# Optimization experiments

Measured on AMD Instinct MI355X. Metric: run time of the kernel, lower is better.

Reference implementation:

```python
import jax, jax.numpy as jnp
import numpy as np

NEG = -1e9


def setup_inputs() -> dict:
    key = jax.random.key(0)
    k1, k2, k3, k4 = jax.random.split(key, 4)
    R, N, D = 64, 200000, 256
    hs = jax.random.normal(k1, (R, D), dtype=jnp.float32)
    es = jax.random.normal(k2, (N, D), dtype=jnp.float32)
    W = jax.random.normal(k3, (D, D), dtype=jnp.float32) / np.sqrt(D)
    mask = jax.random.randint(k4, (R, N), 0, 2) > 0
    return {"hs": hs, "es": es, "W": W, "mask": mask, "n_output": 50}


def reference(hs, es, W, mask, n_output):
    # MatchingLayer: bilinear match scores[r, n] = hs_r^T W es_n  -> [R, N]
    original_scores = (hs @ W) @ es.T
    mu = original_scores.mean()
    std = original_scores.std(ddof=1)  # torch .std() is unbiased
    scores = (original_scores - mu) / std
    # logits used for expansion scores (differentiable)
    logits = jax.nn.log_softmax(scores, axis=-1) + jax.nn.log_softmax(scores, axis=0)
    # detached probabilities for selection
    d = jax.lax.stop_gradient(scores)
    row_probs = jnp.maximum(jax.nn.softmax(jnp.where(mask, d, NEG), axis=-1), 1e-6)
    col_probs = jnp.maximum(jax.nn.softmax(jnp.where(mask, d, NEG), axis=0), 1e-6)
    # deterministic (eval) path: assign each candidate to its argmax category
    index = jnp.argmax(col_probs, axis=0)  # [N]
    R = scores.shape[0]
    valid = mask & (index[None, :] == jnp.arange(R)[:, None])  # [R, N]
    sel = jnp.where(valid, row_probs, -jnp.inf)
    top_vals, top_idx = jax.lax.top_k(sel, n_output)  # [R, n_output]
    ok = jnp.isfinite(top_vals)  # rows with fewer candidates than n_output -> padded
    expansions = jnp.where(ok, top_idx, -1)  # [R, n_output], -1 = pad
    # expansion_scores[i] = logits[:, expansion_i].T -> [n_output, R]
    exp_scores = jnp.transpose(logits[:, top_idx], (1, 2, 0))  # [R, n_output, R]
    exp_scores = exp_scores * ok[:, :, None].astype(exp_scores.dtype)
    return expansions, exp_scores
```

## Files before the change

### kernel.cpp

```cpp
#include <hip/hip_runtime.h>
#include <math.h>

#define RR 64
#define DD 256
#define CAP 6144


__device__ __forceinline__ void get_mu_istd(const double* sums, int N, float& fmu, float& istd) {
  double M = (double)RR * (double)N;
  double mu = sums[0] / M;
  double var = (sums[1] - sums[0] * sums[0] / M) / (M - 1.0);
  fmu = (float)mu;
  istd = (float)(1.0 / sqrt(var));
}

__device__ __forceinline__ void cp16(const void* g, void* l) {
  __builtin_amdgcn_global_load_lds((const __attribute__((address_space(1))) void*)g,
                                   (__attribute__((address_space(3))) void*)l, 16, 0, 0);
}


__global__ __launch_bounds__(256) void k_mask(const void* __restrict__ maskp,
                                              unsigned long long* __restrict__ mbits,
                                              int N) {
  __shared__ int f;
  __shared__ unsigned short pb[4][256];
  int tid = threadIdx.x;
  if (tid == 0) f = 0;
  __syncthreads();
  {
    const unsigned* mw = (const unsigned*)maskp;
    int mode = 0;
    for (int i = tid; i < 4096; i += 256) {
      unsigned v = mw[i];
      if (v == 0x3f800000u) mode = 2;
      else if (v > 1u && mode != 2) mode = 1;
    }
    if (mode) atomicMax(&f, mode);
  }
  __syncthreads();
  const int mode = f;

  const int lane = tid & 63, ty = tid >> 6;
  const int R0 = ty * 16;
  const int n0 = blockIdx.x * 256;
  const int n4 = n0 + lane * 4;
  unsigned g0 = 0, g1 = 0, g2 = 0, g3 = 0;
  const bool vec_ok = (n4 + 3) < N;

  if (mode == 1) {
    const unsigned char* m = (const unsigned char*)maskp;
    if (vec_ok) {
#pragma unroll
      for (int i = 0; i < 16; ++i) {
        uchar4 v = *(const uchar4*)(m + (size_t)(R0 + i) * N + n4);
        g0 |= (unsigned)(v.x != 0) << i;
        g1 |= (unsigned)(v.y != 0) << i;
        g2 |= (unsigned)(v.z != 0) << i;
        g3 |= (unsigned)(v.w != 0) << i;
      }
    } else {
      unsigned* gp[4] = {&g0, &g1, &g2, &g3};
      for (int c = 0; c < 4; ++c)
        if (n4 + c < N)
          for (int i = 0; i < 16; ++i)
            *gp[c] |= (unsigned)(m[(size_t)(R0 + i) * N + n4 + c] != 0) << i;
    }
  } else if (mode == 2) {
    const float* m = (const float*)maskp;
    if (vec_ok) {
#pragma unroll
      for (int i = 0; i < 16; ++i) {
        float4 v = *(const float4*)(m + (size_t)(R0 + i) * N + n4);
        g0 |= (unsigned)(v.x != 0.f) << i;
        g1 |= (unsigned)(v.y != 0.f) << i;
        g2 |= (unsigned)(v.z != 0.f) << i;
        g3 |= (unsigned)(v.w != 0.f) << i;
      }
    } else {
      unsigned* gp[4] = {&g0, &g1, &g2, &g3};
      for (int c = 0; c < 4; ++c)
        if (n4 + c < N)
          for (int i = 0; i < 16; ++i)
            *gp[c] |= (unsigned)(m[(size_t)(R0 + i) * N + n4 + c] != 0.f) << i;
    }
  } else {
    const int* m = (const int*)maskp;
    if (vec_ok) {
#pragma unroll
      for (int i = 0; i < 16; ++i) {
        int4 v = *(const int4*)(m + (size_t)(R0 + i) * N + n4);
        g0 |= (unsigned)(v.x != 0) << i;
        g1 |= (unsigned)(v.y != 0) << i;
        g2 |= (unsigned)(v.z != 0) << i;
        g3 |= (unsigned)(v.w != 0) << i;
      }
    } else {
      unsigned* gp[4] = {&g0, &g1, &g2, &g3};
      for (int c = 0; c < 4; ++c)
        if (n4 + c < N)
          for (int i = 0; i < 16; ++i)
            *gp[c] |= (unsigned)(m[(size_t)(R0 + i) * N + n4 + c] != 0) << i;
    }
  }
  pb[ty][lane * 4 + 0] = (unsigned short)g0;
  pb[ty][lane * 4 + 1] = (unsigned short)g1;
  pb[ty][lane * 4 + 2] = (unsigned short)g2;
  pb[ty][lane * 4 + 3] = (unsigned short)g3;
  __syncthreads();
  const int n = n0 + tid;
  if (n < N) {
    mbits[n] = (unsigned long long)pb[0][tid] |
               ((unsigned long long)pb[1][tid] << 16) |
               ((unsigned long long)pb[2][tid] << 32) |
               ((unsigned long long)pb[3][tid] << 48);
  }
}


__global__ __launch_bounds__(256) void k_hsw(const float* __restrict__ hs,
                                             const float* __restrict__ W,
                                             float* __restrict__ hsW) {
  int i = blockIdx.x;
  int j = threadIdx.x;
  float acc = 0.f;
  for (int k = 0; k < DD; ++k) acc = fmaf(hs[i * DD + k], W[k * DD + j], acc);
  hsW[i * DD + j] = acc;
}


__global__ __launch_bounds__(256) void k_scores(const float* __restrict__ es,
                                                const float* __restrict__ hsW,
                                                const unsigned long long* __restrict__ mbits,
                                                float* __restrict__ scores,
                                                float* __restrict__ colmax,
                                                int* __restrict__ colargmax,
                                                float* __restrict__ qpart,
                                                double* __restrict__ spart,
                                                int N) {
  __shared__ float lds[20480];
  const int tid = threadIdx.x;
  const int lane = tid & 63;
  const int ty = __builtin_amdgcn_readfirstlane(tid >> 6);
  const int n0 = blockIdx.x * 256;
  const int R0 = ty * 16;
  const int nb = n0 + lane;

  const int srow = ty * 8 + (lane >> 3);
  const int sg4 = (((lane & 7) ^ ((lane >> 3) & 7)) << 2);
  const int wrow = ty * 16 + (lane >> 2);
  const int wg4 = (lane & 3) << 2;

  float4 acc[16];
#pragma unroll
  for (int i = 0; i < 16; ++i) acc[i] = make_float4(0.f, 0.f, 0.f, 0.f);

  auto stage = [&](float* ebase, float* wbase, int kc) {
#pragma unroll
    for (int p = 0; p < 8; ++p) {
      const int col = p * 32 + srow;
      const int rr = min(n0 + col, N - 1);
      cp16(es + (size_t)rr * DD + kc + sg4, ebase + p * 1024 + ty * 256);
    }
    cp16(hsW + (size_t)wrow * DD + kc + wg4, wbase + ty * 256);
    cp16(hsW + (size_t)wrow * DD + kc + 16 + wg4, wbase + 1024 + ty * 256);
  };

  stage(lds, lds + 16384, 0);
  asm volatile("s_waitcnt vmcnt(0)" ::: "memory");
  __syncthreads();

  const int swz = (lane & 7);

  for (int kc = 0; kc < DD; kc += 32) {
    const int cur = (kc >> 5) & 1;
    float* ebC = lds + (cur ? 8192 : 0);
    float* wbC = lds + 16384 + (cur ? 2048 : 0);
    if (kc + 32 < DD) {
      float* ebN = lds + (cur ? 0 : 8192);
      float* wbN = lds + 16384 + (cur ? 0 : 2048);
      stage(ebN, wbN, kc + 32);
    }
#pragma unroll
    for (int k = 0; k < 32; k += 4) {
      const int eswz = (((k >> 2) ^ swz) << 2);
      const float4 e0 = *(const float4*)(ebC + (lane       ) * 32 + eswz);
      const float4 e1 = *(const float4*)(ebC + (lane +  64 ) * 32 + eswz);
      const float4 e2 = *(const float4*)(ebC + (lane + 128 ) * 32 + eswz);
      const float4 e3 = *(const float4*)(ebC + (lane + 192 ) * 32 + eswz);
      const float* wk = wbC + ((k >> 4) * 1024) + (k & 15);
#pragma unroll
      for (int i = 0; i < 16; ++i) {
        const float4 w = *(const float4*)(wk + (R0 + i) * 16);
        acc[i].x = fmaf(w.x, e0.x, fmaf(w.y, e0.y, fmaf(w.z, e0.z, fmaf(w.w, e0.w, acc[i].x))));
        acc[i].y = fmaf(w.x, e1.x, fmaf(w.y, e1.y, fmaf(w.z, e1.z, fmaf(w.w, e1.w, acc[i].y))));
        acc[i].z = fmaf(w.x, e2.x, fmaf(w.y, e2.y, fmaf(w.z, e2.z, fmaf(w.w, e2.w, acc[i].z))));
        acc[i].w = fmaf(w.x, e3.x, fmaf(w.y, e3.y, fmaf(w.z, e3.z, fmaf(w.w, e3.w, acc[i].w))));
      }
    }
    asm volatile("s_waitcnt vmcnt(0)" ::: "memory");
    __syncthreads();
  }

  bool val[4];
#pragma unroll
  for (int c = 0; c < 4; ++c) val[c] = (nb + 64 * c) < N;

#pragma unroll
  for (int i = 0; i < 16; ++i) {
    float* dst = scores + (size_t)(R0 + i) * N + nb;
    float v[4] = {acc[i].x, acc[i].y, acc[i].z, acc[i].w};
#pragma unroll
    for (int c = 0; c < 4; ++c)
      if (val[c]) dst[64 * c] = v[c];
  }

  unsigned long long mb[4];
#pragma unroll
  for (int c = 0; c < 4; ++c) mb[c] = val[c] ? mbits[nb + 64 * c] : 0ull;

  float ps1[4], ps2[4], pcm[4], pbv[4];
  int pbr[4];
#pragma unroll
  for (int c = 0; c < 4; ++c) { ps1[c] = 0.f; ps2[c] = 0.f; pcm[c] = -INFINITY; pbv[c] = -INFINITY; pbr[c] = -1; }

#pragma unroll
  for (int i = 0; i < 16; ++i) {
    const int rrow = R0 + i;
    float v[4] = {acc[i].x, acc[i].y, acc[i].z, acc[i].w};
    float q = -INFINITY, qm = -INFINITY;
#pragma unroll
    for (int c = 0; c < 4; ++c) {
      ps1[c] += v[c];
      ps2[c] = fmaf(v[c], v[c], ps2[c]);
      pcm[c] = fmaxf(pcm[c], v[c]);
      bool bit = (mb[c] >> rrow) & 1ull;
      if (bit && (v[c] > pbv[c])) { pbv[c] = v[c]; pbr[c] = rrow; }
      float qv = val[c] ? v[c] : -INFINITY;
      q = fmaxf(q, qv);
      if (bit) qm = fmaxf(qm, qv);
    }
#pragma unroll
    for (int o = 32; o > 0; o >>= 1) {
      q = fmaxf(q, __shfl_down(q, o));
      qm = fmaxf(qm, __shfl_down(qm, o));
    }
    if (lane == 0) {
      qpart[(size_t)blockIdx.x * 128 + rrow] = q;
      qpart[(size_t)blockIdx.x * 128 + 64 + rrow] = qm;
    }
  }

  __syncthreads();
  float* Ls1 = lds;
  float* Ls2 = lds + 1024;
  float* Lcm = lds + 2048;
  float* Lbv = lds + 3072;
  int* Lbr = (int*)(lds + 4096);
  double* red = (double*)(lds + 5120);
#pragma unroll
  for (int c = 0; c < 4; ++c) {
    int col = lane + 64 * c;
    Ls1[ty * 256 + col] = ps1[c];
    Ls2[ty * 256 + col] = ps2[c];
    Lcm[ty * 256 + col] = pcm[c];
    Lbv[ty * 256 + col] = pbv[c];
    Lbr[ty * 256 + col] = pbr[c];
  }
  __syncthreads();

  const int n = n0 + tid;
  float s1 = 0.f, s2 = 0.f;
  if (n < N) {
    s1 = Ls1[tid] + Ls1[256 + tid] + Ls1[512 + tid] + Ls1[768 + tid];
    s2 = Ls2[tid] + Ls2[256 + tid] + Ls2[512 + tid] + Ls2[768 + tid];
    float cm = fmaxf(fmaxf(Lcm[tid], Lcm[256 + tid]), fmaxf(Lcm[512 + tid], Lcm[768 + tid]));
    colmax[n] = cm;
    float bv = -INFINITY;
    int br = -1;
#pragma unroll
    for (int w2 = 0; w2 < 4; ++w2) {
      float b = Lbv[w2 * 256 + tid];
      if (b > bv) { bv = b; br = Lbr[w2 * 256 + tid]; }
    }
    colargmax[n] = br;
  }

  double d1 = (double)s1, d2 = (double)s2;
#pragma unroll
  for (int o = 32; o > 0; o >>= 1) {
    d1 += __shfl_down(d1, o);
    d2 += __shfl_down(d2, o);
  }
  if ((tid & 63) == 0) { red[ty * 2] = d1; red[ty * 2 + 1] = d2; }
  __syncthreads();
  if (tid == 0) {
    spart[(size_t)blockIdx.x * 2] = red[0] + red[2] + red[4] + red[6];
    spart[(size_t)blockIdx.x * 2 + 1] = red[1] + red[3] + red[5] + red[7];
  }
}


__global__ __launch_bounds__(256) void k_redfuse(const float* __restrict__ qpart,
                                                 const double* __restrict__ spart,
                                                 float* __restrict__ rowmaxf,
                                                 double* __restrict__ sums,
                                                 int* __restrict__ cnt,
                                                 int NBlk) {
  const int tid = threadIdx.x, lane = tid & 63, ty = tid >> 6;
  if (blockIdx.x < 128) {
    const int slot = blockIdx.x;
    __shared__ float w[4];
    float m = -INFINITY;
    for (int i = tid; i < NBlk; i += 256) m = fmaxf(m, qpart[(size_t)i * 128 + slot]);
#pragma unroll
    for (int o = 32; o > 0; o >>= 1) m = fmaxf(m, __shfl_down(m, o));
    if (lane == 0) w[ty] = m;
    __syncthreads();
    if (tid == 0) rowmaxf[slot] = fmaxf(fmaxf(w[0], w[1]), fmaxf(w[2], w[3]));
  } else {
    __shared__ double r[8];
    double s0 = 0.0, s1 = 0.0;
    for (int i = tid; i < NBlk; i += 256) {
      s0 += spart[(size_t)i * 2];
      s1 += spart[(size_t)i * 2 + 1];
    }
#pragma unroll
    for (int o = 32; o > 0; o >>= 1) {
      s0 += __shfl_down(s0, o);
      s1 += __shfl_down(s1, o);
    }
    if (lane == 0) { r[ty * 2] = s0; r[ty * 2 + 1] = s1; }
    if (tid < RR) cnt[tid] = 0;
    __syncthreads();
    if (tid == 0) {
      sums[0] = r[0] + r[2] + r[4] + r[6];
      sums[1] = r[1] + r[3] + r[5] + r[7];
    }
  }
}


__global__ __launch_bounds__(256) void k_colpass(const float* __restrict__ scores,
                                                 const float* __restrict__ colmax,
                                                 const int* __restrict__ colargmax,
                                                 const unsigned long long* __restrict__ mbits,
                                                 const double* __restrict__ sums,
                                                 const float* __restrict__ rowmaxf,
                                                 float* __restrict__ collse,
                                                 float* __restrict__ colpart,
                                                 int* __restrict__ cnt,
                                                 float* __restrict__ candx,
                                                 int* __restrict__ candn,
                                                 int N) {
  __shared__ float rmS[64], suS[64], smS[64];
  __shared__ float rowU[64], rowM[64];
  __shared__ float cpart[4][256];
  __shared__ int lcnt[64], lbase[64];
  const int tid = threadIdx.x, lane = tid & 63, ty = tid >> 6;
  const int R0 = ty * 16;
  float fmu, istd;
  get_mu_istd(sums, N, fmu, istd);
  if (tid < 64) {
    rmS[tid] = rowmaxf[tid];
    lcnt[tid] = 0;
  }
  __syncthreads();
  float gm = rmS[0];
#pragma unroll
  for (int r = 1; r < RR; ++r) gm = fmaxf(gm, rmS[r]);
  if (tid < 64) {
    suS[tid] = expf((gm - rmS[tid]) * istd);
    smS[tid] = expf((gm - rowmaxf[64 + tid]) * istd);
  }

  const int n0 = blockIdx.x * 256;
  const int n4 = n0 + lane * 4;
  bool vc[4];
  unsigned mbr[4];
#pragma unroll
  for (int c = 0; c < 4; ++c) {
    vc[c] = (n4 + c) < N;
    unsigned long long mw = vc[c] ? mbits[n4 + c] : 0ull;
    mbr[c] = (unsigned)((mw >> R0) & 0xffffull);
  }

  float cs0 = 0.f, cs1 = 0.f, cs2 = 0.f, cs3 = 0.f;
#pragma unroll
  for (int i = 0; i < 16; ++i) {
    const int r = R0 + i;
    const float4 x = *(const float4*)(scores + (size_t)r * N + n4);
    float E0 = vc[0] ? expf((x.x - gm) * istd) : 0.f;
    float E1 = vc[1] ? expf((x.y - gm) * istd) : 0.f;
    float E2 = vc[2] ? expf((x.z - gm) * istd) : 0.f;
    float E3 = vc[3] ? expf((x.w - gm) * istd) : 0.f;
    cs0 += E0; cs1 += E1; cs2 += E2; cs3 += E3;
    float eu = (E0 + E1) + (E2 + E3);
    float em = (((mbr[0] >> i) & 1u) ? E0 : 0.f) + (((mbr[1] >> i) & 1u) ? E1 : 0.f) +
               (((mbr[2] >> i) & 1u) ? E2 : 0.f) + (((mbr[3] >> i) & 1u) ? E3 : 0.f);
#pragma unroll
    for (int o = 32; o > 0; o >>= 1) {
      eu += __shfl_down(eu, o);
      em += __shfl_down(em, o);
    }
    if (lane == 0) { rowU[r] = eu; rowM[r] = em; }
  }

  cpart[ty][lane * 4 + 0] = cs0;
  cpart[ty][lane * 4 + 1] = cs1;
  cpart[ty][lane * 4 + 2] = cs2;
  cpart[ty][lane * 4 + 3] = cs3;
  __syncthreads();

  const int n = n0 + tid;
  const bool valid = n < N;
  int br = -1;
  if (valid) {
    float colsum = ((cpart[0][tid] + cpart[1][tid]) + cpart[2][tid]) + cpart[3][tid];
    collse[n] = logf(colsum) + (gm - colmax[n]) * istd;
    br = colargmax[n];
  }
  int lpos = 0;
  if (br >= 0) lpos = atomicAdd(&lcnt[br], 1);
  __syncthreads();
  if (tid < 64) {
    colpart[(size_t)blockIdx.x * 128 + tid] = rowU[tid] * suS[tid];
    colpart[(size_t)blockIdx.x * 128 + 64 + tid] = rowM[tid] * smS[tid];
    int c = lcnt[tid];
    lbase[tid] = c ? atomicAdd(&cnt[tid], c) : 0;
  }
  __syncthreads();
  if (br >= 0) {
    int pos = lbase[br] + lpos;
    if (pos < CAP) {
      candx[(size_t)br * CAP + pos] = scores[(size_t)br * N + n];
      candn[(size_t)br * CAP + pos] = n;
    }
  }
}


__global__ __launch_bounds__(256) void k_redacc(const float* __restrict__ colpart,
                                                const float* __restrict__ rowmaxf,
                                                float* __restrict__ rowstats,
                                                int NBlk) {
  const int slot = blockIdx.x;
  const int tid = threadIdx.x, lane = tid & 63, ty = tid >> 6;
  __shared__ float w[4];
  float s = 0.f;
  for (int i = tid; i < NBlk; i += 256) s += colpart[(size_t)i * 128 + slot];
#pragma unroll
  for (int o = 32; o > 0; o >>= 1) s += __shfl_down(s, o);
  if (lane == 0) w[ty] = s;
  __syncthreads();
  if (tid == 0) {
    float total = w[0] + w[1] + w[2] + w[3];
    if (slot < 64) {
      rowstats[slot] = rowmaxf[slot];
      rowstats[64 + slot] = logf(total);
    } else {
      rowstats[128 + (slot - 64)] = rowmaxf[slot];
      rowstats[192 + (slot - 64)] = total;
    }
  }
}


__global__ __launch_bounds__(512) void k_topkx(const int* __restrict__ cnt,
                                               const float* __restrict__ candx,
                                               const int* __restrict__ candn,
                                               const double* __restrict__ sums,
                                               const float* __restrict__ rowstats,
                                               const float* __restrict__ scores,
                                               const float* __restrict__ colmax,
                                               const float* __restrict__ collse,
                                               float* __restrict__ out,
                                               int N, int NO) {
  int r = blockIdx.x, tid = threadIdx.x;
  __shared__ float sp[CAP];
  __shared__ int sn[CAP];
  __shared__ float wp[8];
  __shared__ int wn[8], wi[8];
  __shared__ int selS[64];
  int c = min(cnt[r], CAP);
  float fmu, istd;
  get_mu_istd(sums, N, fmu, istd);
  const float rmm = rowstats[128 + r];
  const float lm = rowstats[192 + r];
  for (int i = tid; i < c; i += 512) {
    float xv = candx[(size_t)r * CAP + i];
    sp[i] = fmaxf(expf((xv - rmm) * istd) / lm, 1e-6f);
    sn[i] = candn[(size_t)r * CAP + i];
  }
  __syncthreads();
  for (int j = 0; j < NO; ++j) {
    float bp = -1.f;
    int bn = 0x7fffffff, bi = -1;
    for (int i = tid; i < c; i += 512) {
      float p = sp[i];
      int nn = sn[i];
      if (p > bp || (p == bp && nn < bn)) { bp = p; bn = nn; bi = i; }
    }
#pragma unroll
    for (int o = 32; o > 0; o >>= 1) {
      float p2 = __shfl_down(bp, o);
      int n2 = __shfl_down(bn, o);
      int i2 = __shfl_down(bi, o);
      if (p2 > bp || (p2 == bp && n2 < bn)) { bp = p2; bn = n2; bi = i2; }
    }
    if ((tid & 63) == 0) { wp[tid >> 6] = bp; wn[tid >> 6] = bn; wi[tid >> 6] = bi; }
    __syncthreads();
    if (tid == 0) {
      float fp2 = wp[0]; int fn2 = wn[0], fi2 = wi[0];
#pragma unroll
      for (int w2 = 1; w2 < 8; ++w2) {
        if (wp[w2] > fp2 || (wp[w2] == fp2 && wn[w2] < fn2)) { fp2 = wp[w2]; fn2 = wn[w2]; fi2 = wi[w2]; }
      }
      if (fp2 > 0.f) {
        out[r * NO + j] = (float)fn2;
        selS[j] = fn2;
        sp[fi2] = -1.f;
      } else {
        out[r * NO + j] = -1.f;
        selS[j] = -1;
      }
    }
    __syncthreads();
  }

  for (int idx = tid; idx < NO * RR; idx += 512) {
    const int j = idx >> 6;
    const int r2 = idx & 63;
    const int n = selS[j];
    float v = 0.f;
    if (n >= 0) {
      float x = scores[(size_t)r2 * N + n];
      float v1 = (x - rowstats[r2]) * istd - rowstats[64 + r2];
      float v2 = (x - colmax[n]) * istd - collse[n];
      v = v1 + v2;
    }
    out[RR * NO + ((size_t)r * NO + j) * RR + r2] = v;
  }
}


extern "C" void kernel_launch(void* const* d_in, const int* in_sizes, int n_in,
                              void* d_out, int out_size, void* d_ws, size_t ws_size,
                              hipStream_t stream) {
  const float* hs = (const float*)d_in[0];
  const float* es = (const float*)d_in[1];
  const float* W = (const float*)d_in[2];
  const void* mask = d_in[3];

  const int N = in_sizes[1] / DD;
  const int NO = out_size / (RR * (1 + RR));
  const int NB = (N + 255) / 256;

  char* ws = (char*)d_ws;
  size_t o = 0;
  float* scores = (float*)(ws + o);   o += (size_t)RR * N * 4;
  float* hsW = (float*)(ws + o);      o += RR * DD * 4;
  o = (o + 255) & ~(size_t)255;
  double* sums = (double*)(ws + o);
  int* cnt = (int*)(ws + o + 16);
  o += 512;
  float* rowstats = (float*)(ws + o); o += 256 * 4;
  float* rowmaxf = (float*)(ws + o);  o += 128 * 4;
  o = (o + 255) & ~(size_t)255;
  float* colmax = (float*)(ws + o);   o += (size_t)N * 4;
  int* colargmax = (int*)(ws + o);    o += (size_t)N * 4;
  float* collse = (float*)(ws + o);   o += (size_t)N * 4;
  o = (o + 255) & ~(size_t)255;
  unsigned long long* mbits = (unsigned long long*)(ws + o); o += (size_t)N * 8;
  o = (o + 255) & ~(size_t)255;
  float* candx = (float*)(ws + o);    o += (size_t)RR * CAP * 4;
  int* candn = (int*)(ws + o);        o += (size_t)RR * CAP * 4;
  o = (o + 255) & ~(size_t)255;
  float* qpart = (float*)(ws + o);    o += (size_t)NB * 128 * 4;
  double* spart = (double*)(ws + o);  o += (size_t)NB * 2 * 8;
  float* colpart = (float*)(ws + o);  o += (size_t)NB * 128 * 4;

  k_mask<<<NB, 256, 0, stream>>>(mask, mbits, N);
  k_hsw<<<RR, 256, 0, stream>>>(hs, W, hsW);
  k_scores<<<NB, 256, 0, stream>>>(es, hsW, mbits, scores, colmax, colargmax,
                                   qpart, spart, N);
  k_redfuse<<<129, 256, 0, stream>>>(qpart, spart, rowmaxf, sums, cnt, NB);
  k_colpass<<<NB, 256, 0, stream>>>(scores, colmax, colargmax, mbits, sums, rowmaxf,
                                    collse, colpart, cnt, candx, candn, N);
  k_redacc<<<128, 256, 0, stream>>>(colpart, rowmaxf, rowstats, NB);
  k_topkx<<<RR, 512, 0, stream>>>(cnt, candx, candn, sums, rowstats, scores, colmax,
                                  collse, (float*)d_out, N, NO);
}
```

Measured before the change: 590.6 us.

## Fuse mask bit-packing into scores kernel and widen it to 512 threads

Drops the separate mask-packing kernel and does the mask read and bit-packing inside the scores kernel, so the packed bits come from shared memory instead of a second global pass. The scores kernel goes from 256 to 512 threads, each wave now handling 8 rows instead of 16, which halves per-thread accumulators to improve occupancy and latency hiding. Per-block partials (qpart, colpart) are switched to a slot-major layout so the reduction kernels read them contiguously. The trade-off is more threads sharing the same LDS tiles and an extra block-wide sync for the mask packing.

Result: faster. 573.3 us (-2.9%).

```diff
diff --git a/kernel.cpp b/kernel.cpp
--- a/kernel.cpp
+++ b/kernel.cpp
@@ -17,104 +17,6 @@
 __device__ __forceinline__ void cp16(const void* g, void* l) {
   __builtin_amdgcn_global_load_lds((const __attribute__((address_space(1))) void*)g,
                                    (__attribute__((address_space(3))) void*)l, 16, 0, 0);
-}
-
-
-__global__ __launch_bounds__(256) void k_mask(const void* __restrict__ maskp,
-                                              unsigned long long* __restrict__ mbits,
-                                              int N) {
-  __shared__ int f;
-  __shared__ unsigned short pb[4][256];
-  int tid = threadIdx.x;
-  if (tid == 0) f = 0;
-  __syncthreads();
-  {
-    const unsigned* mw = (const unsigned*)maskp;
-    int mode = 0;
-    for (int i = tid; i < 4096; i += 256) {
-      unsigned v = mw[i];
-      if (v == 0x3f800000u) mode = 2;
-      else if (v > 1u && mode != 2) mode = 1;
-    }
-    if (mode) atomicMax(&f, mode);
-  }
-  __syncthreads();
-  const int mode = f;
-
-  const int lane = tid & 63, ty = tid >> 6;
-  const int R0 = ty * 16;
-  const int n0 = blockIdx.x * 256;
-  const int n4 = n0 + lane * 4;
-  unsigned g0 = 0, g1 = 0, g2 = 0, g3 = 0;
-  const bool vec_ok = (n4 + 3) < N;
-
-  if (mode == 1) {
-    const unsigned char* m = (const unsigned char*)maskp;
-    if (vec_ok) {
-#pragma unroll
-      for (int i = 0; i < 16; ++i) {
-        uchar4 v = *(const uchar4*)(m + (size_t)(R0 + i) * N + n4);
-        g0 |= (unsigned)(v.x != 0) << i;
-        g1 |= (unsigned)(v.y != 0) << i;
-        g2 |= (unsigned)(v.z != 0) << i;
-        g3 |= (unsigned)(v.w != 0) << i;
-      }
-    } else {
-      unsigned* gp[4] = {&g0, &g1, &g2, &g3};
-      for (int c = 0; c < 4; ++c)
-        if (n4 + c < N)
-          for (int i = 0; i < 16; ++i)
-            *gp[c] |= (unsigned)(m[(size_t)(R0 + i) * N + n4 + c] != 0) << i;
-    }
-  } else if (mode == 2) {
-    const float* m = (const float*)maskp;
-    if (vec_ok) {
-#pragma unroll
-      for (int i = 0; i < 16; ++i) {
-        float4 v = *(const float4*)(m + (size_t)(R0 + i) * N + n4);
-        g0 |= (unsigned)(v.x != 0.f) << i;
-        g1 |= (unsigned)(v.y != 0.f) << i;
-        g2 |= (unsigned)(v.z != 0.f) << i;
-        g3 |= (unsigned)(v.w != 0.f) << i;
-      }
-    } else {
-      unsigned* gp[4] = {&g0, &g1, &g2, &g3};
-      for (int c = 0; c < 4; ++c)
-        if (n4 + c < N)
-          for (int i = 0; i < 16; ++i)
-            *gp[c] |= (unsigned)(m[(size_t)(R0 + i) * N + n4 + c] != 0.f) << i;
-    }
-  } else {
-    const int* m = (const int*)maskp;
-    if (vec_ok) {
-#pragma unroll
-      for (int i = 0; i < 16; ++i) {
-        int4 v = *(const int4*)(m + (size_t)(R0 + i) * N + n4);
-        g0 |= (unsigned)(v.x != 0) << i;
-        g1 |= (unsigned)(v.y != 0) << i;
-        g2 |= (unsigned)(v.z != 0) << i;
-        g3 |= (unsigned)(v.w != 0) << i;
-      }
-    } else {
-      unsigned* gp[4] = {&g0, &g1, &g2, &g3};
-      for (int c = 0; c < 4; ++c)
-        if (n4 + c < N)
-          for (int i = 0; i < 16; ++i)
-            *gp[c] |= (unsigned)(m[(size_t)(R0 + i) * N + n4 + c] != 0) << i;
-    }
-  }
-  pb[ty][lane * 4 + 0] = (unsigned short)g0;
-  pb[ty][lane * 4 + 1] = (unsigned short)g1;
-  pb[ty][lane * 4 + 2] = (unsigned short)g2;
-  pb[ty][lane * 4 + 3] = (unsigned short)g3;
-  __syncthreads();
-  const int n = n0 + tid;
-  if (n < N) {
-    mbits[n] = (unsigned long long)pb[0][tid] |
-               ((unsigned long long)pb[1][tid] << 16) |
-               ((unsigned long long)pb[2][tid] << 32) |
-               ((unsigned long long)pb[3][tid] << 48);
-  }
 }
 
 
@@ -129,46 +31,62 @@
 }
 
 
-__global__ __launch_bounds__(256) void k_scores(const float* __restrict__ es,
-                                                const float* __restrict__ hsW,
-                                                const unsigned long long* __restrict__ mbits,
-                                                float* __restrict__ scores,
-                                                float* __restrict__ colmax,
-                                                int* __restrict__ colargmax,
-                                                float* __restrict__ qpart,
-                                                double* __restrict__ spart,
-                                                int N) {
+__global__ __launch_bounds__(512, 4) void k_scores(const float* __restrict__ es,
+                                                   const float* __restrict__ hsW,
+                                                   const void* __restrict__ maskp,
+                                                   unsigned long long* __restrict__ mbits,
+                                                   float* __restrict__ scores,
+                                                   float* __restrict__ colmax,
+                                                   int* __restrict__ colargmax,
+                                                   float* __restrict__ qpart,
+                                                   double* __restrict__ spart,
+                                                   int N) {
   __shared__ float lds[20480];
   const int tid = threadIdx.x;
   const int lane = tid & 63;
   const int ty = __builtin_amdgcn_readfirstlane(tid >> 6);
   const int n0 = blockIdx.x * 256;
-  const int R0 = ty * 16;
+  const int NBg = gridDim.x;
+  const int R0 = ty * 8;
   const int nb = n0 + lane;
 
-  const int srow = ty * 8 + (lane >> 3);
+  int* fS = (int*)(lds + 15000);
+  unsigned char* pb = (unsigned char*)(lds + 14336);
+
+  if (tid == 0) *fS = 0;
+
   const int sg4 = (((lane & 7) ^ ((lane >> 3) & 7)) << 2);
-  const int wrow = ty * 16 + (lane >> 2);
-  const int wg4 = (lane & 3) << 2;
-
-  float4 acc[16];
-#pragma unroll
-  for (int i = 0; i < 16; ++i) acc[i] = make_float4(0.f, 0.f, 0.f, 0.f);
+  const int wrow = (tid >> 2) & 63;
+  const int whalf = tid >> 8;
+  const int wg4 = (tid & 3) << 2;
+
+  float4 acc[8];
+#pragma unroll
+  for (int i = 0; i < 8; ++i) acc[i] = make_float4(0.f, 0.f, 0.f, 0.f);
 
   auto stage = [&](float* ebase, float* wbase, int kc) {
 #pragma unroll
-    for (int p = 0; p < 8; ++p) {
-      const int col = p * 32 + srow;
+    for (int p = 0; p < 4; ++p) {
+      const int col = p * 64 + (tid >> 3);
       const int rr = min(n0 + col, N - 1);
-      cp16(es + (size_t)rr * DD + kc + sg4, ebase + p * 1024 + ty * 256);
-    }
-    cp16(hsW + (size_t)wrow * DD + kc + wg4, wbase + ty * 256);
-    cp16(hsW + (size_t)wrow * DD + kc + 16 + wg4, wbase + 1024 + ty * 256);
+      cp16(es + (size_t)rr * DD + kc + sg4, ebase + p * 2048 + ty * 256);
+    }
+    cp16(hsW + (size_t)wrow * DD + kc + whalf * 16 + wg4, wbase + ty * 256);
   };
 
   stage(lds, lds + 16384, 0);
+  int mymode = 0;
+  {
+    const unsigned* mw = (const unsigned*)maskp;
+    for (int i = tid; i < 4096; i += 512) {
+      unsigned v = mw[i];
+      if (v == 0x3f800000u) mymode = 2;
+      else if (v > 1u && mymode != 2) mymode = 1;
+    }
+  }
   asm volatile("s_waitcnt vmcnt(0)" ::: "memory");
   __syncthreads();
+  if (mymode) atomicMax(fS, mymode);
 
   const int swz = (lane & 7);
 
@@ -190,7 +108,7 @@
       const float4 e3 = *(const float4*)(ebC + (lane + 192 ) * 32 + eswz);
       const float* wk = wbC + ((k >> 4) * 1024) + (k & 15);
 #pragma unroll
-      for (int i = 0; i < 16; ++i) {
+      for (int i = 0; i < 8; ++i) {
         const float4 w = *(const float4*)(wk + (R0 + i) * 16);
         acc[i].x = fmaf(w.x, e0.x, fmaf(w.y, e0.y, fmaf(w.z, e0.z, fmaf(w.w, e0.w, acc[i].x))));
         acc[i].y = fmaf(w.x, e1.x, fmaf(w.y, e1.y, fmaf(w.z, e1.z, fmaf(w.w, e1.w, acc[i].y))));
@@ -207,7 +125,7 @@
   for (int c = 0; c < 4; ++c) val[c] = (nb + 64 * c) < N;
 
 #pragma unroll
-  for (int i = 0; i < 16; ++i) {
+  for (int i = 0; i < 8; ++i) {
     float* dst = scores + (size_t)(R0 + i) * N + nb;
     float v[4] = {acc[i].x, acc[i].y, acc[i].z, acc[i].w};
 #pragma unroll
@@ -215,9 +133,87 @@
       if (val[c]) dst[64 * c] = v[c];
   }
 
-  unsigned long long mb[4];
-#pragma unroll
-  for (int c = 0; c < 4; ++c) mb[c] = val[c] ? mbits[nb + 64 * c] : 0ull;
+  const int mode = *fS;
+  {
+    const int n4 = n0 + lane * 4;
+    unsigned g0 = 0, g1 = 0, g2 = 0, g3 = 0;
+    const bool vec_ok = (n4 + 3) < N;
+    if (mode == 1) {
+      const unsigned char* m = (const unsigned char*)maskp;
+      if (vec_ok) {
+#pragma unroll
+        for (int i = 0; i < 8; ++i) {
+          uchar4 v = *(const uchar4*)(m + (size_t)(R0 + i) * N + n4);
+          g0 |= (unsigned)(v.x != 0) << i;
+          g1 |= (unsigned)(v.y != 0) << i;
+          g2 |= (unsigned)(v.z != 0) << i;
+          g3 |= (unsigned)(v.w != 0) << i;
+        }
+      } else {
+        unsigned* gp[4] = {&g0, &g1, &g2, &g3};
+        for (int c = 0; c < 4; ++c)
+          if (n4 + c < N)
+            for (int i = 0; i < 8; ++i)
+              *gp[c] |= (unsigned)(m[(size_t)(R0 + i) * N + n4 + c] != 0) << i;
+      }
+    } else if (mode == 2) {
+      const float* m = (const float*)maskp;
+      if (vec_ok) {
+#pragma unroll
+        for (int i = 0; i < 8; ++i) {
+          float4 v = *(const float4*)(m + (size_t)(R0 + i) * N + n4);
+          g0 |= (unsigned)(v.x != 0.f) << i;
+          g1 |= (unsigned)(v.y != 0.f) << i;
+          g2 |= (unsigned)(v.z != 0.f) << i;
+          g3 |= (unsigned)(v.w != 0.f) << i;
+        }
+      } else {
+        unsigned* gp[4] = {&g0, &g1, &g2, &g3};
+        for (int c = 0; c < 4; ++c)
+          if (n4 + c < N)
+            for (int i = 0; i < 8; ++i)
+              *gp[c] |= (unsigned)(m[(size_t)(R0 + i) * N + n4 + c] != 0.f) << i;
+      }
+    } else {
+      const int* m = (const int*)maskp;
+      if (vec_ok) {
+#pragma unroll
+        for (int i = 0; i < 8; ++i) {
+          int4 v = *(const int4*)(m + (size_t)(R0 + i) * N + n4);
+          g0 |= (unsigned)(v.x != 0) << i;
+          g1 |= (unsigned)(v.y != 0) << i;
+          g2 |= (unsigned)(v.z != 0) << i;
+          g3 |= (unsigned)(v.w != 0) << i;
+        }
+      } else {
+        unsigned* gp[4] = {&g0, &g1, &g2, &g3};
+        for (int c = 0; c < 4; ++c)
+          if (n4 + c < N)
+            for (int i = 0; i < 8; ++i)
+              *gp[c] |= (unsigned)(m[(size_t)(R0 + i) * N + n4 + c] != 0) << i;
+      }
+    }
+    pb[ty * 256 + lane * 4 + 0] = (unsigned char)g0;
+    pb[ty * 256 + lane * 4 + 1] = (unsigned char)g1;
+    pb[ty * 256 + lane * 4 + 2] = (unsigned char)g2;
+    pb[ty * 256 + lane * 4 + 3] = (unsigned char)g3;
+  }
+  __syncthreads();
+
+  if (tid < 256) {
+    const int n = n0 + tid;
+    if (n < N) {
+      unsigned long long b = 0;
+#pragma unroll
+      for (int w2 = 0; w2 < 8; ++w2)
+        b |= (unsigned long long)pb[w2 * 256 + tid] << (8 * w2);
+      mbits[n] = b;
+    }
+  }
+
+  unsigned mbr[4];
+#pragma unroll
+  for (int c = 0; c < 4; ++c) mbr[c] = pb[ty * 256 + lane + 64 * c];
 
   float ps1[4], ps2[4], pcm[4], pbv[4];
   int pbr[4];
@@ -225,7 +221,7 @@
   for (int c = 0; c < 4; ++c) { ps1[c] = 0.f; ps2[c] = 0.f; pcm[c] = -INFINITY; pbv[c] = -INFINITY; pbr[c] = -1; }
 
 #pragma unroll
-  for (int i = 0; i < 16; ++i) {
+  for (int i = 0; i < 8; ++i) {
     const int rrow = R0 + i;
     float v[4] = {acc[i].x, acc[i].y, acc[i].z, acc[i].w};
     float q = -INFINITY, qm = -INFINITY;
@@ -234,7 +230,7 @@
       ps1[c] += v[c];
       ps2[c] = fmaf(v[c], v[c], ps2[c]);
       pcm[c] = fmaxf(pcm[c], v[c]);
-      bool bit = (mb[c] >> rrow) & 1ull;
+      bool bit = (mbr[c] >> i) & 1u;
       if (bit && (v[c] > pbv[c])) { pbv[c] = v[c]; pbr[c] = rrow; }
       float qv = val[c] ? v[c] : -INFINITY;
       q = fmaxf(q, qv);
@@ -246,18 +242,18 @@
       qm = fmaxf(qm, __shfl_down(qm, o));
     }
     if (lane == 0) {
-      qpart[(size_t)blockIdx.x * 128 + rrow] = q;
-      qpart[(size_t)blockIdx.x * 128 + 64 + rrow] = qm;
+      qpart[(size_t)rrow * NBg + blockIdx.x] = q;
+      qpart[(size_t)(64 + rrow) * NBg + blockIdx.x] = qm;
     }
   }
 
   __syncthreads();
   float* Ls1 = lds;
-  float* Ls2 = lds + 1024;
-  float* Lcm = lds + 2048;
-  float* Lbv = lds + 3072;
-  int* Lbr = (int*)(lds + 4096);
-  double* red = (double*)(lds + 5120);
+  float* Ls2 = lds + 2048;
+  float* Lcm = lds + 4096;
+  float* Lbv = lds + 6144;
+  int* Lbr = (int*)(lds + 8192);
+  double* red = (double*)(lds + 10240);
 #pragma unroll
   for (int c = 0; c < 4; ++c) {
     int col = lane + 64 * c;
@@ -269,21 +265,23 @@
   }
   __syncthreads();
 
-  const int n = n0 + tid;
   float s1 = 0.f, s2 = 0.f;
-  if (n < N) {
-    s1 = Ls1[tid] + Ls1[256 + tid] + Ls1[512 + tid] + Ls1[768 + tid];
-    s2 = Ls2[tid] + Ls2[256 + tid] + Ls2[512 + tid] + Ls2[768 + tid];
-    float cm = fmaxf(fmaxf(Lcm[tid], Lcm[256 + tid]), fmaxf(Lcm[512 + tid], Lcm[768 + tid]));
-    colmax[n] = cm;
-    float bv = -INFINITY;
-    int br = -1;
-#pragma unroll
-    for (int w2 = 0; w2 < 4; ++w2) {
-      float b = Lbv[w2 * 256 + tid];
-      if (b > bv) { bv = b; br = Lbr[w2 * 256 + tid]; }
-    }
-    colargmax[n] = br;
+  if (tid < 256) {
+    const int n = n0 + tid;
+    if (n < N) {
+      float cm = -INFINITY, bv = -INFINITY;
+      int br = -1;
+#pragma unroll
+      for (int w2 = 0; w2 < 8; ++w2) {
+        s1 += Ls1[w2 * 256 + tid];
+        s2 += Ls2[w2 * 256 + tid];
+        cm = fmaxf(cm, Lcm[w2 * 256 + tid]);
+        float b = Lbv[w2 * 256 + tid];
+        if (b > bv) { bv = b; br = Lbr[w2 * 256 + tid]; }
+      }
+      colmax[n] = cm;
+      colargmax[n] = br;
+    }
   }
 
   double d1 = (double)s1, d2 = (double)s2;
@@ -292,11 +290,14 @@
     d1 += __shfl_down(d1, o);
     d2 += __shfl_down(d2, o);
   }
-  if ((tid & 63) == 0) { red[ty * 2] = d1; red[ty * 2 + 1] = d2; }
+  if (lane == 0) { red[ty * 2] = d1; red[ty * 2 + 1] = d2; }
   __syncthreads();
   if (tid == 0) {
-    spart[(size_t)blockIdx.x * 2] = red[0] + red[2] + red[4] + red[6];
-    spart[(size_t)blockIdx.x * 2 + 1] = red[1] + red[3] + red[5] + red[7];
+    double t1 = 0.0, t2 = 0.0;
+#pragma unroll
+    for (int w2 = 0; w2 < 8; ++w2) { t1 += red[w2 * 2]; t2 += red[w2 * 2 + 1]; }
+    spart[(size_t)blockIdx.x * 2] = t1;
+    spart[(size_t)blockIdx.x * 2 + 1] = t2;
   }
 }
 
@@ -312,7 +313,7 @@
     const int slot = blockIdx.x;
     __shared__ float w[4];
     float m = -INFINITY;
-    for (int i = tid; i < NBlk; i += 256) m = fmaxf(m, qpart[(size_t)i * 128 + slot]);
+    for (int i = tid; i < NBlk; i += 256) m = fmaxf(m, qpart[(size_t)slot * NBlk + i]);
 #pragma unroll
     for (int o = 32; o > 0; o >>= 1) m = fmaxf(m, __shfl_down(m, o));
     if (lane == 0) w[ty] = m;
@@ -359,6 +360,7 @@
   __shared__ int lcnt[64], lbase[64];
   const int tid = threadIdx.x, lane = tid & 63, ty = tid >> 6;
   const int R0 = ty * 16;
+  const int NBg = gridDim.x;
   float fmu, istd;
   get_mu_istd(sums, N, fmu, istd);
   if (tid < 64) {
@@ -424,8 +426,8 @@
   if (br >= 0) lpos = atomicAdd(&lcnt[br], 1);
   __syncthreads();
   if (tid < 64) {
-    colpart[(size_t)blockIdx.x * 128 + tid] = rowU[tid] * suS[tid];
-    colpart[(size_t)blockIdx.x * 128 + 64 + tid] = rowM[tid] * smS[tid];
+    colpart[(size_t)tid * NBg + blockIdx.x] = rowU[tid] * suS[tid];
+    colpart[(size_t)(64 + tid) * NBg + blockIdx.x] = rowM[tid] * smS[tid];
     int c = lcnt[tid];
     lbase[tid] = c ? atomicAdd(&cnt[tid], c) : 0;
   }
@@ -448,7 +450,7 @@
   const int tid = threadIdx.x, lane = tid & 63, ty = tid >> 6;
   __shared__ float w[4];
   float s = 0.f;
-  for (int i = tid; i < NBlk; i += 256) s += colpart[(size_t)i * 128 + slot];
+  for (int i = tid; i < NBlk; i += 256) s += colpart[(size_t)slot * NBlk + i];
 #pragma unroll
   for (int o = 32; o > 0; o >>= 1) s += __shfl_down(s, o);
   if (lane == 0) w[ty] = s;
@@ -580,9 +582,8 @@
   double* spart = (double*)(ws + o);  o += (size_t)NB * 2 * 8;
   float* colpart = (float*)(ws + o);  o += (size_t)NB * 128 * 4;
 
-  k_mask<<<NB, 256, 0, stream>>>(mask, mbits, N);
   k_hsw<<<RR, 256, 0, stream>>>(hs, W, hsW);
-  k_scores<<<NB, 256, 0, stream>>>(es, hsW, mbits, scores, colmax, colargmax,
+  k_scores<<<NB, 512, 0, stream>>>(es, hsW, mask, mbits, scores, colmax, colargmax,
                                    qpart, spart, N);
   k_redfuse<<<129, 256, 0, stream>>>(qpart, spart, rowmaxf, sums, cnt, NB);
   k_colpass<<<NB, 256, 0, stream>>>(scores, colmax, colargmax, mbits, sums, rowmaxf,
```
